# Kernel optimization log

Measured on AMD Instinct MI355X. Metric: run time of the kernel, lower is better.

The kernel has to match this reference:

```python
import jax, jax.numpy as jnp
import numpy as np

H = 256          # encoder hidden per direction
D = 2 * H        # decoder hidden / bidirectional feature dim
IN = 2
OUT = 2
B = 64
T = 256
STEPS = 24       # hard-coded decoder loop length in the source


def gru_cell(x, h, Wih, Whh, bih, bhh):
    # PyTorch GRU cell: gate order (r, z, n)
    gi = x @ Wih.T + bih
    gh = h @ Whh.T + bhh
    ir, iz, inn = jnp.split(gi, 3, axis=-1)
    hr, hz, hn = jnp.split(gh, 3, axis=-1)
    r = jax.nn.sigmoid(ir + hr)
    z = jax.nn.sigmoid(iz + hz)
    n = jnp.tanh(inn + r * hn)
    return (1.0 - z) * n + z * h


def run_dir(xs, Wih, Whh, bih, bhh, reverse):
    # xs: (T, B, F) time-major; returns outputs (T, B, H) and last hidden (B, H)
    h0 = jnp.zeros((xs.shape[1], Whh.shape[-1]), xs.dtype)
    def step(h, xt):
        h2 = gru_cell(xt, h, Wih, Whh, bih, bhh)
        return h2, h2
    h_last, ys = jax.lax.scan(step, h0, xs, reverse=reverse)
    return ys, h_last


def setup_inputs():
    keys = jax.random.split(jax.random.key(0), 24)
    k = iter(keys)
    def rn(shape, s):
        return jax.random.normal(next(k), shape, jnp.float32) * s
    se = 1.0 / np.sqrt(H)
    sd = 1.0 / np.sqrt(D)
    return {
        "x": rn((B, T, IN), 1.0),
        "enc_Wih0": rn((2, 3 * H, IN), se),
        "enc_Whh0": rn((2, 3 * H, H), se),
        "enc_bih0": rn((2, 3 * H), se),
        "enc_bhh0": rn((2, 3 * H), se),
        "enc_Wih": rn((2, 2, 3 * H, D), se),
        "enc_Whh": rn((2, 2, 3 * H, H), se),
        "enc_bih": rn((2, 2, 3 * H), se),
        "enc_bhh": rn((2, 2, 3 * H), se),
        "dec_Wih": rn((3, 3 * D, D), sd),
        "dec_Whh": rn((3, 3 * D, D), sd),
        "dec_bih": rn((3, 3 * D), sd),
        "dec_bhh": rn((3, 3 * D), sd),
        "fc_con_W": rn((D, 2 * D), sd),
        "fc_con_b": rn((D,), sd),
        "attn_W": rn((D, 2 * D), sd),
        "attn_b": rn((D,), sd),
        "v": jax.random.uniform(next(k), (D,), jnp.float32),  # torch.rand init
        "fc_W": rn((OUT, D), sd),
        "fc_b": rn((OUT,), sd),
    }


def reference(x, enc_Wih0, enc_Whh0, enc_bih0, enc_bhh0,
              enc_Wih, enc_Whh, enc_bih, enc_bhh,
              dec_Wih, dec_Whh, dec_bih, dec_bhh,
              fc_con_W, fc_con_b, attn_W, attn_b, v, fc_W, fc_b):
    # ---- bidirectional 3-layer GRU encoder ----
    seq = x.transpose(1, 0, 2)  # (T, B, IN) time-major
    hf_list, hb_list = [], []
    for l in range(3):
        if l == 0:
            Wf, Uf, bf, cf = enc_Wih0[0], enc_Whh0[0], enc_bih0[0], enc_bhh0[0]
            Wb, Ub, bb, cb = enc_Wih0[1], enc_Whh0[1], enc_bih0[1], enc_bhh0[1]
        else:
            Wf, Uf, bf, cf = enc_Wih[l-1, 0], enc_Whh[l-1, 0], enc_bih[l-1, 0], enc_bhh[l-1, 0]
            Wb, Ub, bb, cb = enc_Wih[l-1, 1], enc_Whh[l-1, 1], enc_bih[l-1, 1], enc_bhh[l-1, 1]
        yf, hf = run_dir(seq, Wf, Uf, bf, cf, False)
        yb, hb = run_dir(seq, Wb, Ub, bb, cb, True)
        seq = jnp.concatenate([yf, yb], axis=-1)
        hf_list.append(hf)
        hb_list.append(hb)
    enc_out = seq.transpose(1, 0, 2)  # (B, T, D)
    # hidden_decoder = cat(forward, backward) per layer -> (3, B, D)
    hidden = jnp.stack([jnp.concatenate([f, b], axis=-1)
                        for f, b in zip(hf_list, hb_list)])
    dec_in = enc_out[:, -1, :]  # (B, D)

    # additive attention: energy = tanh(W [h; enc_out] + b); precompute enc part
    attn_Wh = attn_W[:, :D]
    attn_We = attn_W[:, D:]
    enc_proj = jnp.einsum('bte,de->btd', enc_out, attn_We)  # (B, T, D)

    def dec_step(carry, _):
        d_in, hid = carry
        hq = hid[-1] @ attn_Wh.T                               # (B, D)
        energy = jnp.tanh(hq[:, None, :] + enc_proj + attn_b)  # (B, T, D)
        scores = jnp.einsum('btd,d->bt', energy, v)
        aw = jax.nn.softmax(scores, axis=1)                    # (B, T)
        ctx = jnp.einsum('bt,btd->bd', aw, enc_out)            # (B, D)
        inp = jnp.concatenate([d_in, ctx], axis=-1) @ fc_con_W.T + fc_con_b
        new_h = []
        for l in range(3):  # 3-layer unidirectional decoder GRU, single step
            hl = gru_cell(inp, hid[l], dec_Wih[l], dec_Whh[l], dec_bih[l], dec_bhh[l])
            new_h.append(hl)
            inp = hl
        out_step = inp @ fc_W.T + fc_b
        return (inp, jnp.stack(new_h)), out_step

    _, outs = jax.lax.scan(dec_step, (dec_in, hidden), None, length=STEPS)
    return outs.transpose(1, 0, 2)  # (B, 24, OUT)
```

## Files before the change

### kernel.cpp

```cpp
#include <hip/hip_runtime.h>

typedef unsigned short u16;
typedef unsigned int u32;
typedef _Float16 f16;
typedef f16   f16x2 __attribute__((ext_vector_type(2)));
typedef f16   f16x4 __attribute__((ext_vector_type(4)));
typedef f16   f16x8 __attribute__((ext_vector_type(8)));
typedef float f32x4 __attribute__((ext_vector_type(4)));

#define MFMA16(a,b,c) __builtin_amdgcn_mfma_f32_16x16x32_f16((a),(b),(c),0,0,0)

__device__ __forceinline__ float sigm_(float x){ return 1.f/(1.f + __expf(-x)); }
__device__ __forceinline__ float tanh_(float x){ return 1.f - 2.f/(1.f + __expf(2.f*x)); }
__device__ __forceinline__ float clampf(float x, float c){
  if (!(x > -c)) x = -c;
  if (x > c) x = c;
  return x;
}
__device__ __forceinline__ f16x8 cvt8f(const float* p){
  const float4 a = *(const float4*)p;
  const float4 b = *(const float4*)(p+4);
  f16x8 r;
  r[0]=(f16)a.x; r[1]=(f16)a.y; r[2]=(f16)a.z; r[3]=(f16)a.w;
  r[4]=(f16)b.x; r[5]=(f16)b.y; r[6]=(f16)b.z; r[7]=(f16)b.w;
  return r;
}

__device__ __forceinline__ void gbar8_(u32* c){
  __syncthreads();
  __threadfence();
  if (threadIdx.x == 0) {
    __hip_atomic_fetch_add(c, 1u, __ATOMIC_RELAXED, __HIP_MEMORY_SCOPE_AGENT);
    while (__hip_atomic_load(c, __ATOMIC_RELAXED, __HIP_MEMORY_SCOPE_AGENT) < 8u)
      __builtin_amdgcn_s_sleep(2);
  }
  __syncthreads();
  __threadfence();
}

__global__ void k_diag(float* out, int mib){
  const int i = blockIdx.x*256 + threadIdx.x;
  if (i < 3072) out[i] = 1000.f * (float)mib;
}

__global__ void k_prep_dec(const float* dWhh, const float* attnW, const float* fccon,
                           const float* dWih, f16* R3)
{
  long idx = (long)blockIdx.x*256 + threadIdx.x;
  const float* src; int rs, colOff = 0, NKS; long dst, loc;
  if (idx < 294912L) {
    loc = idx; const int m = (int)(loc / 98304); loc %= 98304;
    src = dWhh + (long)m*786432; rs = 512; NKS = 16; dst = (long)m*786432;
  } else if (idx < 327680L) {
    loc = idx - 294912L; src = attnW; colOff = 512; rs = 1024; NKS = 16; dst = 2359296L;
  } else if (idx < 393216L) {
    loc = idx - 327680L; src = fccon; rs = 1024; NKS = 32; dst = 2621440L;
  } else if (idx < 688128L) {
    loc = idx - 393216L; const int m = (int)(loc / 98304); loc %= 98304;
    src = dWih + (long)m*786432; rs = 512; NKS = 16; dst = 3440640L + (long)m*786432;
  } else if (idx < 720896L) {
    loc = idx - 688128L; src = attnW; colOff = 0; rs = 1024; NKS = 16; dst = 5799936L;
  } else return;
  const int lane = (int)(loc & 63);
  const long frag = loc >> 6;
  const int ks = (int)(frag % NKS);
  const long nt = frag / NKS;
  const int n  = (int)(nt*16 + (lane & 15));
  const int k0 = ks*32 + ((lane >> 4) << 3);
  const float* sp = src + (long)n*rs + colOff + k0;
  f16* dp = R3 + dst + loc*8;
  #pragma unroll
  for (int j = 0; j < 8; ++j) dp[j] = (f16)sp[j];
}

__global__ void k_gi0s(const float* __restrict__ x, const float* __restrict__ W,
                       const float* __restrict__ bi, f16* __restrict__ gi,
                       int seg, int BH, int lbh, int b0)
{
  const long idx = (long)blockIdx.x*256 + threadIdx.x;
  const int v = (int)(idx % 24);
  long rest = idx / 24;
  const int tid = (int)(rest & 511); rest >>= 9;
  const int bq = (int)(rest & ((1 << (lbh-4)) - 1)); rest >>= (lbh-4);
  const int s = (int)(rest & 63);
  const int d = (int)(rest >> 6);
  const int r = v / 6, rem = v % 6, i = rem / 3, g = rem % 3;
  const int w = tid >> 6, q = (tid >> 4) & 3, lo = tid & 15;
  const int n = g*256 + (2*w + i)*16 + lo;
  const int b = bq*16 + q*4 + r;
  const int t = d ? (255 - (seg*64 + s)) : (seg*64 + s);
  const float x0 = x[(((b0+b)<<8) + t)*2];
  const float x1 = x[(((b0+b)<<8) + t)*2 + 1];
  const long wi = ((long)d*768 + n)*2;
  gi[idx] = (f16)clampf(x0*W[wi] + x1*W[wi+1] + bi[d*768 + n], 32.f);
}

#define GIE(G, vv) ((float)((vv) < 8 ? (G)[0][(vv)&7] : ((vv) < 16 ? (G)[1][(vv)-8] : (G)[2][(vv)-16])))

__global__ __launch_bounds__(512, 1) void k_enc_seg(
    const f16* __restrict__ gi, const float* __restrict__ Wraw,
    const float* __restrict__ bhh, f16* __restrict__ seq, int ostr,
    f16* __restrict__ fin, float* __restrict__ hcar, int seg, int BH)
{
  const int tid = threadIdx.x;
  const int w = tid >> 6, lane = tid & 63;
  const int lo16 = lane & 15, quad = lane >> 4;
  const int nbq = BH >> 4;
  const int dir = blockIdx.x / nbq, bq = blockIdx.x % nbq;

  __shared__ f16 h16[4][16][264];

  const float* mat = Wraw + (long)dir*196608;
  f16x8 wr[6][8];
  #pragma unroll
  for (int p = 0; p < 3; ++p)
    #pragma unroll
    for (int i = 0; i < 2; ++i) {
      const int n = (p*16 + 2*w + i)*16 + lo16;
      #pragma unroll
      for (int ks = 0; ks < 8; ++ks)
        wr[p*2+i][ks] = cvt8f(mat + (long)n*256 + ks*32 + quad*8);
    }
  float bh_[3][2];
  #pragma unroll
  for (int p = 0; p < 3; ++p)
    #pragma unroll
    for (int i = 0; i < 2; ++i)
      bh_[p][i] = bhh[dir*768 + p*256 + (2*w+i)*16 + lo16];

  float hreg[2][4];
  if (seg == 0) {
    #pragma unroll
    for (int i = 0; i < 2; ++i)
      #pragma unroll
      for (int r = 0; r < 4; ++r) {
        hreg[i][r] = 0.f;
        h16[0][quad*4 + r][(2*w+i)*16 + lo16] = (f16)0.f;
      }
  } else {
    #pragma unroll
    for (int i = 0; i < 2; ++i) {
      const int c = (2*w+i)*16 + lo16;
      #pragma unroll
      for (int r = 0; r < 4; ++r) {
        const float v = hcar[((dir*BH) + bq*16 + quad*4 + r)*256 + c];
        hreg[i][r] = v;
        h16[0][quad*4 + r][c] = (f16)v;
      }
    }
  }

  const long gstep = (long)nbq*512*24;
  const f16* gbase = gi + (((long)dir*64*nbq + bq)*512 + tid)*24;
  f16x8 g0[3], g1[3];
  { const f16x8* gp = (const f16x8*)gbase; g0[0]=gp[0]; g0[1]=gp[1]; g0[2]=gp[2]; }

  const int frow = tid >> 5;
  const int fcol = (tid & 31) * 8;

  for (int s = 0; s < 64; ++s) {
    __syncthreads();
    if (s >= 2) {
      const int so = s - 2;
      const int t2 = dir ? (255 - (seg*64 + so)) : (seg*64 + so);
      const f16x8 hv = *(const f16x8*)&h16[(so+1)&3][frow][fcol];
      *(f16x8*)&seq[((long)t2*ostr + bq*16 + frow)*512 + dir*256 + fcol] = hv;
    }
    f32x4 acc[6];
    #pragma unroll
    for (int q = 0; q < 6; ++q) acc[q] = (f32x4){0.f,0.f,0.f,0.f};
    #pragma unroll
    for (int ks = 0; ks < 8; ++ks) {
      const f16x8 a = *(const f16x8*)&h16[s&3][lo16][ks*32 + quad*8];
      #pragma unroll
      for (int q = 0; q < 6; ++q)
        acc[q] = MFMA16(a, wr[q][ks], acc[q]);
    }
    if (s < 63) {
      const f16x8* gp = (const f16x8*)(gbase + (long)(s+1)*gstep);
      g1[0]=gp[0]; g1[1]=gp[1]; g1[2]=gp[2];
    }
    #pragma unroll
    for (int i = 0; i < 2; ++i) {
      const int c = (2*w+i)*16 + lo16;
      #pragma unroll
      for (int r = 0; r < 4; ++r) {
        const int row = quad*4 + r;
        const int v = r*6 + i*3;
        const float gir = GIE(g0, v);
        const float giz = GIE(g0, v+1);
        const float gin = GIE(g0, v+2);
        const float rv = sigm_(gir + acc[i][r]   + bh_[0][i]);
        const float zv = sigm_(giz + acc[2+i][r] + bh_[1][i]);
        const float nv = tanh_(gin + rv*(acc[4+i][r] + bh_[2][i]));
        float hn = (1.f - zv)*nv + zv*hreg[i][r];
        hn = clampf(hn, 2.f);
        hreg[i][r] = hn;
        h16[(s+1)&3][row][c] = (f16)hn;
        if (seg == 3 && s == 63) fin[(bq*16 + row)*512 + dir*256 + c] = (f16)hn;
      }
    }
    g0[0]=g1[0]; g0[1]=g1[1]; g0[2]=g1[2];
  }
  __syncthreads();
  #pragma unroll
  for (int so = 62; so < 64; ++so) {
    const int t2 = dir ? (255 - (seg*64 + so)) : (seg*64 + so);
    const f16x8 hv = *(const f16x8*)&h16[(so+1)&3][frow][fcol];
    *(f16x8*)&seq[((long)t2*ostr + bq*16 + frow)*512 + dir*256 + fcol] = hv;
  }
  #pragma unroll
  for (int i = 0; i < 2; ++i) {
    const int c = (2*w+i)*16 + lo16;
    #pragma unroll
    for (int r = 0; r < 4; ++r)
      hcar[((dir*BH) + bq*16 + quad*4 + r)*256 + c] = hreg[i][r];
  }
}

__global__ void k_gemm_gi(const f16* __restrict__ A,
                          const float* __restrict__ Braw, long bzs,
                          const float* __restrict__ bias,
                          f16* __restrict__ gi,
                          int tb0, int tb1, int tdirsgn, int abstr, float cv)
{
  const int tid = threadIdx.x, w = tid>>6, lane = tid&63;
  const int lo16 = lane&15, quad = lane>>4;
  const int s_ = blockIdx.x;
  const int y  = blockIdx.y;
  const int z  = blockIdx.z;
  const int tbase = z ? tb1 : tb0;
  const int tdir  = z ? -tdirsgn : tdirsgn;
  const int mrow = s_*64 + w*16 + lo16;
  const long arow = (long)(tbase + tdir*(mrow >> 6))*abstr + (mrow & 63);
  const f16* Ap = A + arow*512 + quad*8;
  const float* Bp = Braw + (long)z*bzs;
  f32x4 acc[12];
  #pragma unroll
  for (int i=0;i<12;++i) acc[i]=(f32x4){0.f,0.f,0.f,0.f};
  for (int ks = 0; ks < 16; ++ks) {
    const f16x8 a = *(const f16x8*)(Ap + ks*32);
    #pragma unroll
    for (int g = 0; g < 3; ++g)
      #pragma unroll
      for (int jj = 0; jj < 4; ++jj) {
        const int n = g*256 + y*64 + jj*16 + lo16;
        const f16x8 b = cvt8f(Bp + (long)n*512 + ks*32 + quad*8);
        acc[g*4+jj] = MFMA16(a, b, acc[g*4+jj]);
      }
  }
  f16* base = gi + (((long)z*64 + s_)*4 + w)*12288L;
  #pragma unroll
  for (int l = 0; l < 2; ++l) {
    f16x8 rec8[3];
    #pragma unroll
    for (int r = 0; r < 4; ++r)
      #pragma unroll
      for (int jl = 0; jl < 2; ++jl)
        #pragma unroll
        for (int g = 0; g < 3; ++g) {
          const int nt = g*4 + l*2 + jl;
          const int n = g*256 + y*64 + (l*2+jl)*16 + lo16;
          const int slot = r*6 + jl*3 + g;
          rec8[slot>>3][slot&7] = (f16)clampf(acc[nt][r] + bias[z*768 + n], cv);
        }
    f16* dp = base + ((long)(y*2 + l)*64 + quad*16 + lo16)*24L;
    *(f16x8*)(dp)      = rec8[0];
    *(f16x8*)(dp + 8)  = rec8[1];
    *(f16x8*)(dp + 16) = rec8[2];
  }
}

__global__ void k_gemm(const f16* __restrict__ A, int K,
                       const f16* __restrict__ Bsw, const float* __restrict__ Braw,
                       long bzs, int ldb, int koff,
                       const float* __restrict__ bias, int biaszs,
                       void* __restrict__ Cv, long czs, int ldc, int mode,
                       int tb0, int tb1, int tdirsgn, int lbh, int abstr, float cv)
{
  const int tid = threadIdx.x, w = tid>>6, lane = tid&63;
  const int lo16 = lane&15, quad = lane>>4;
  const int m0 = blockIdx.x*64 + w*16;
  const int n0 = blockIdx.y*128;
  const int z  = blockIdx.z;
  const int tbase = z ? tb1 : tb0;
  const int tdir  = z ? -tdirsgn : tdirsgn;
  const int NKS = K >> 5;
  const int mrow = m0 + lo16;
  const long arow = (long)(tbase + tdir*(mrow >> lbh))*abstr + (mrow & ((1<<lbh)-1));
  const f16* Ap = A + arow*K + quad*8;
  f32x4 acc[8];
  #pragma unroll
  for (int i=0;i<8;++i) acc[i]=(f32x4){0.f,0.f,0.f,0.f};
  if (Bsw) {
    const f16* Bp = Bsw + (long)z*bzs;
    for (int ks = 0; ks < NKS; ++ks) {
      const f16x8 a = *(const f16x8*)(Ap + ks*32);
      #pragma unroll
      for (int nt = 0; nt < 8; ++nt) {
        const f16x8 b = *(const f16x8*)(Bp + (((long)((n0>>4)+nt)*NKS + ks) << 9) + lane*8);
        acc[nt] = MFMA16(a, b, acc[nt]);
      }
    }
  } else {
    const float* Bp = Braw + (long)z*bzs;
    for (int ks = 0; ks < NKS; ++ks) {
      const f16x8 a = *(const f16x8*)(Ap + ks*32);
      #pragma unroll
      for (int nt = 0; nt < 8; ++nt) {
        const f16x8 b = cvt8f(Bp + (long)(n0 + nt*16 + lo16)*ldb + koff + ks*32 + quad*8);
        acc[nt] = MFMA16(a, b, acc[nt]);
      }
    }
  }
  #pragma unroll
  for (int nt = 0; nt < 8; ++nt) {
    const int n = n0 + nt*16 + lo16;
    const float bv = bias ? bias[z*biaszs + n] : 0.f;
    #pragma unroll
    for (int r = 0; r < 4; ++r) {
      const int m = m0 + quad*4 + r;
      const float val = clampf(acc[nt][r] + bv, cv);
      if (mode == 2) {
        const int s_ = m >> lbh, b_ = m & ((1<<lbh)-1);
        const int bq_ = b_ >> 4, q_ = (b_ >> 2) & 3, r_ = b_ & 3;
        const int g_ = n >> 8, j_ = (n >> 4) & 15, lo_ = n & 15;
        const long idx = ((((long)z*64 + s_)*(1<<(lbh-4)) + bq_)*512
                          + ((j_>>1)*64 + q_*16 + lo_))*24 + r_*6 + (j_&1)*3 + g_;
        ((f16*)Cv)[idx] = (f16)val;
      } else if (mode == 3)
        ((f16*)Cv)[(((long)(m & 63) << 8) + (m >> 6))*512 + n] = (f16)val;
      else if (mode == 1)
        ((f16*)Cv)[(long)z*czs + (long)m*ldc + n] = (f16)val;
      else
        ((float*)Cv)[(long)z*czs + (long)m*ldc + n] = val;
    }
  }
}

__global__ void k_score(const f16* __restrict__ seq, const f16* __restrict__ We,
                        const float* __restrict__ hq, const float* __restrict__ ab,
                        const float* __restrict__ vp, float* __restrict__ S)
{
  const int t = blockIdx.x, tid = threadIdx.x;
  const int w = tid>>6, lane = tid&63, lo16 = lane&15, quad = lane>>4;
  __shared__ float svab[1024];
  for (int i = tid; i < 512; i += 256) { svab[i] = vp[i]; svab[512+i] = ab[i]; }
  __syncthreads();
  f32x4 acc[32];
  #pragma unroll
  for (int i=0;i<32;++i) acc[i]=(f32x4){0.f,0.f,0.f,0.f};
  const f16* Ap = seq + ((long)t*64 + w*16 + lo16)*512 + quad*8;
  for (int ks = 0; ks < 16; ++ks) {
    const f16x8 a = *(const f16x8*)(Ap + ks*32);
    #pragma unroll
    for (int nt = 0; nt < 32; ++nt) {
      const f16x8 b = *(const f16x8*)(We + (((long)nt*16 + ks) << 9) + lane*8);
      acc[nt] = MFMA16(a, b, acc[nt]);
    }
  }
  #pragma unroll
  for (int r = 0; r < 4; ++r) {
    const int b = w*16 + quad*4 + r;
    float sc = 0.f;
    #pragma unroll
    for (int nt = 0; nt < 32; ++nt) {
      const int n = nt*16 + lo16;
      sc += svab[n] * tanh_(acc[nt][r] + hq[(b<<9) + n] + svab[512+n]);
    }
    sc += __shfl_xor(sc, 1, 64); sc += __shfl_xor(sc, 2, 64);
    sc += __shfl_xor(sc, 4, 64); sc += __shfl_xor(sc, 8, 64);
    if (lo16 == 0) S[(b<<8) + t] = clampf(sc, 256.f);
  }
}

__global__ void k_attnctx(const float* __restrict__ S, const f16* __restrict__ enc,
                          f16* __restrict__ cat)
{
  const int b = blockIdx.x, tid = threadIdx.x;
  __shared__ float ssc[256], srd[256];
  const float sc = clampf(S[(b<<8) + tid], 256.f);
  srd[tid] = sc; __syncthreads();
  for (int off = 128; off > 0; off >>= 1) { if (tid < off) srd[tid] = fmaxf(srd[tid], srd[tid+off]); __syncthreads(); }
  const float mx = srd[0]; __syncthreads();
  const float e = __expf(sc - mx);
  srd[tid] = e; __syncthreads();
  for (int off = 128; off > 0; off >>= 1) { if (tid < off) srd[tid] += srd[tid+off]; __syncthreads(); }
  const float inv = 1.f / srd[0]; __syncthreads();
  ssc[tid] = e * inv; __syncthreads();
  float c0 = 0.f, c1 = 0.f;
  for (int tt = 0; tt < 256; ++tt) {
    const float awt = ssc[tt];
    const f16* ep = enc + (((long)tt*64 + b) << 9);
    c0 += awt * (float)ep[tid];
    c1 += awt * (float)ep[256 + tid];
  }
  cat[(b<<10) + 512 + tid] = (f16)clampf(c0, 4.f);
  cat[(b<<10) + 768 + tid] = (f16)clampf(c1, 4.f);
}

__global__ void k_dec_init(const f16* __restrict__ fin, const f16* __restrict__ seq,
                           f16* __restrict__ hb16, float* __restrict__ hf32,
                           f16* __restrict__ cat, u32* __restrict__ cnt)
{
  const int idx = blockIdx.x*256 + threadIdx.x;
  if (idx < 3072) cnt[idx] = 0;
  const int d = idx & 511, b = (idx >> 9) & 63, l = idx >> 15;
  if (l < 3) {
    const float v = clampf((float)fin[((long)l<<15) + (b<<9) + d], 2.f);
    hb16[(long)l*65536 + (b<<9) + d] = (f16)v;
    hf32[(long)l*32768 + (b<<9) + d] = v;
  } else {
    cat[(b<<10) + d] = seq[((long)255*64 + b)*512 + d];
  }
}

__global__ __launch_bounds__(512, 1) void k_attn(
    const f16* __restrict__ seq, const f16* __restrict__ ep,
    const float* __restrict__ hf2, const f16* __restrict__ cat,
    const f16* __restrict__ whsw, const f16* __restrict__ fcsw,
    const float* __restrict__ fcconB, const float* __restrict__ vp,
    f16* __restrict__ inp, const float* __restrict__ fcW,
    const float* __restrict__ fcb, float* __restrict__ out, int step)
{
  const int b = blockIdx.x;
  const int tid = threadIdx.x, w = tid >> 6, lane = tid & 63;
  const int quad = lane >> 4;
  __shared__ float hsm[512];
  __shared__ float cats[1024];
  __shared__ float hqs[512];
  __shared__ float aw[256];
  __shared__ float red[8*512];
  hsm[tid]  = hf2[(b<<9) + tid];
  cats[tid] = (float)cat[(b<<10) + tid];
  __syncthreads();
  if (w < 2 && step > 0) {
    float p = 0.f;
    #pragma unroll
    for (int j = 0; j < 8; ++j) p += fcW[(w<<9) + lane*8 + j] * hsm[lane*8 + j];
    p += __shfl_xor(p,1,64); p += __shfl_xor(p,2,64); p += __shfl_xor(p,4,64);
    p += __shfl_xor(p,8,64); p += __shfl_xor(p,16,64); p += __shfl_xor(p,32,64);
    if (lane == 0) out[(b*24 + step-1)*2 + w] = clampf(p + fcb[w], 128.f);
  }
  #pragma unroll
  for (int i = 0; i < 4; ++i) {
    const int nt = w*4 + i;
    float p = 0.f;
    for (int ks = 0; ks < 16; ++ks) {
      const f16x8 wv = *(const f16x8*)(whsw + (((long)nt*16 + ks)<<9) + lane*8);
      const float4 ha = *(const float4*)&hsm[ks*32 + quad*8];
      const float4 hb = *(const float4*)&hsm[ks*32 + quad*8 + 4];
      p += (float)wv[0]*ha.x + (float)wv[1]*ha.y + (float)wv[2]*ha.z + (float)wv[3]*ha.w
         + (float)wv[4]*hb.x + (float)wv[5]*hb.y + (float)wv[6]*hb.z + (float)wv[7]*hb.w;
    }
    p += __shfl_xor(p,16,64); p += __shfl_xor(p,32,64);
    if (lane < 16) hqs[nt*16 + lane] = p;
  }
  __syncthreads();
  float hq8[8], v8[8];
  #pragma unroll
  for (int j = 0; j < 8; ++j) { hq8[j] = hqs[lane*8+j]; v8[j] = vp[lane*8+j]; }
  #pragma unroll 2
  for (int i = 0; i < 32; ++i) {
    const int t = w*32 + i;
    const f16x8 e = *(const f16x8*)(ep + (((long)(b<<8) + t)<<9) + lane*8);
    float s = 0.f;
    #pragma unroll
    for (int j = 0; j < 8; ++j) s += v8[j]*tanh_((float)e[j] + hq8[j]);
    s += __shfl_xor(s,1,64); s += __shfl_xor(s,2,64); s += __shfl_xor(s,4,64);
    s += __shfl_xor(s,8,64); s += __shfl_xor(s,16,64); s += __shfl_xor(s,32,64);
    if (lane == 0) aw[t] = clampf(s, 256.f);
  }
  __syncthreads();
  if (tid < 64) {
    float s0=aw[tid], s1=aw[tid+64], s2=aw[tid+128], s3=aw[tid+192];
    float mx = fmaxf(fmaxf(s0,s1), fmaxf(s2,s3));
    mx = fmaxf(mx, __shfl_xor(mx,1,64)); mx = fmaxf(mx, __shfl_xor(mx,2,64));
    mx = fmaxf(mx, __shfl_xor(mx,4,64)); mx = fmaxf(mx, __shfl_xor(mx,8,64));
    mx = fmaxf(mx, __shfl_xor(mx,16,64)); mx = fmaxf(mx, __shfl_xor(mx,32,64));
    const float e0=__expf(s0-mx), e1=__expf(s1-mx), e2=__expf(s2-mx), e3=__expf(s3-mx);
    float sm = e0+e1+e2+e3;
    sm += __shfl_xor(sm,1,64); sm += __shfl_xor(sm,2,64); sm += __shfl_xor(sm,4,64);
    sm += __shfl_xor(sm,8,64); sm += __shfl_xor(sm,16,64); sm += __shfl_xor(sm,32,64);
    const float inv = 1.f/sm;
    aw[tid]=e0*inv; aw[tid+64]=e1*inv; aw[tid+128]=e2*inv; aw[tid+192]=e3*inv;
  }
  __syncthreads();
  float c8[8];
  #pragma unroll
  for (int j = 0; j < 8; ++j) c8[j] = 0.f;
  #pragma unroll 2
  for (int i = 0; i < 32; ++i) {
    const int t = w*32 + i;
    const f16x8 e = *(const f16x8*)(seq + (((long)t*64 + b)<<9) + lane*8);
    const float awt = aw[t];
    #pragma unroll
    for (int j = 0; j < 8; ++j) c8[j] += awt*(float)e[j];
  }
  #pragma unroll
  for (int j = 0; j < 8; ++j) red[(w<<9) + lane*8 + j] = c8[j];
  __syncthreads();
  {
    float s = 0.f;
    #pragma unroll
    for (int ww = 0; ww < 8; ++ww) s += red[(ww<<9) + tid];
    cats[512 + tid] = clampf(s, 4.f);
  }
  __syncthreads();
  #pragma unroll
  for (int i = 0; i < 4; ++i) {
    const int nt = w*4 + i;
    float p = 0.f;
    for (int ks = 0; ks < 32; ++ks) {
      const f16x8 wv = *(const f16x8*)(fcsw + (((long)nt*32 + ks)<<9) + lane*8);
      const float4 ca = *(const float4*)&cats[ks*32 + quad*8];
      const float4 cb = *(const float4*)&cats[ks*32 + quad*8 + 4];
      p += (float)wv[0]*ca.x + (float)wv[1]*ca.y + (float)wv[2]*ca.z + (float)wv[3]*ca.w
         + (float)wv[4]*cb.x + (float)wv[5]*cb.y + (float)wv[6]*cb.z + (float)wv[7]*cb.w;
    }
    p += __shfl_xor(p,16,64); p += __shfl_xor(p,32,64);
    if (lane < 16) inp[(b<<9) + nt*16 + lane] = (f16)clampf(p + fcconB[nt*16+lane], 64.f);
  }
}

__global__ void k_cell3(const f16* __restrict__ inp0, const f16* __restrict__ WihSw,
                        const f16* __restrict__ WhhSw, const float* __restrict__ bihA,
                        const float* __restrict__ bhhA, float* __restrict__ hfA,
                        f16* __restrict__ hb, f16* __restrict__ cat, int p, u32* cnt)
{
  const int tid = threadIdx.x, w = tid>>6, lane = tid&63;
  const int lo16 = lane&15, quad = lane>>4;
  const int Wt = ((int)blockIdx.x & 7)*4 + w;
  const int mi = (int)blockIdx.x >> 3;
  for (int l = 0; l < 3; ++l) {
    const f16* inp = (l == 0) ? inp0 : (hb + (long)(2*(l-1) + (1-p))*32768);
    const f16* WihL = WihSw + (long)l*786432;
    const f16* WhhL = WhhSw + (long)l*786432;
    const float* bih = bihA + l*1536;
    const float* bhh = bhhA + l*1536;
    float* hf32 = hfA + (long)l*32768;
    const f16* hin = hb + (long)(2*l + p)*32768;
    f16* hout = hb + (long)(2*l + (1-p))*32768;
    f16* catp = (l == 2) ? cat : (f16*)nullptr;

    f32x4 arz[2], an_[2];
    #pragma unroll
    for (int i=0;i<2;++i){ arz[i]=(f32x4){0.f,0.f,0.f,0.f}; an_[i]=(f32x4){0.f,0.f,0.f,0.f}; }
    #pragma unroll 4
    for (int kk = 0; kk < 16; ++kk) {
      const f16x8 b0 = *(const f16x8*)(WihL + (((long)Wt*16 + kk)<<9)      + lane*8);
      const f16x8 b1 = *(const f16x8*)(WihL + (((long)(32+Wt)*16 + kk)<<9) + lane*8);
      const f16x8 b2 = *(const f16x8*)(WihL + (((long)(64+Wt)*16 + kk)<<9) + lane*8);
      const f16x8 a = *(const f16x8*)&inp[((mi*16 + lo16)<<9) + kk*32 + quad*8];
      arz[0] = MFMA16(a, b0, arz[0]);
      arz[1] = MFMA16(a, b1, arz[1]);
      an_[0] = MFMA16(a, b2, an_[0]);
    }
    #pragma unroll 4
    for (int kk = 0; kk < 16; ++kk) {
      const f16x8 b0 = *(const f16x8*)(WhhL + (((long)Wt*16 + kk)<<9)      + lane*8);
      const f16x8 b1 = *(const f16x8*)(WhhL + (((long)(32+Wt)*16 + kk)<<9) + lane*8);
      const f16x8 b2 = *(const f16x8*)(WhhL + (((long)(64+Wt)*16 + kk)<<9) + lane*8);
      const f16x8 a = *(const f16x8*)&hin[((mi*16 + lo16)<<9) + kk*32 + quad*8];
      arz[0] = MFMA16(a, b0, arz[0]);
      arz[1] = MFMA16(a, b1, arz[1]);
      an_[1] = MFMA16(a, b2, an_[1]);
    }
    const int c = Wt*16 + lo16;
    const float brz0 = bih[c]     + bhh[c];
    const float brz1 = bih[512+c] + bhh[512+c];
    const float bin_ = bih[1024+c];
    const float bhn_ = bhh[1024+c];
    #pragma unroll
    for (int r = 0; r < 4; ++r) {
      const int row = mi*16 + quad*4 + r;
      const float rv = sigm_(clampf(arz[0][r],64.f) + brz0);
      const float zv = sigm_(clampf(arz[1][r],64.f) + brz1);
      const float nv = tanh_(clampf(an_[0][r],64.f) + bin_ + rv*(clampf(an_[1][r],64.f) + bhn_));
      const float ho = hf32[(row<<9) + c];
      float hn2 = (1.f - zv)*nv + zv*ho;
      hn2 = clampf(hn2, 2.f);
      hf32[(row<<9) + c] = hn2;
      hout[(row<<9) + c] = (f16)hn2;
      if (catp) catp[(row<<10) + c] = (f16)hn2;
    }
    if (l < 2) gbar8_(cnt + (l*4 + mi)*16);
  }
}

__global__ void k_cell_raw(const f16* __restrict__ inp, const float* __restrict__ WihRaw,
                           const f16* __restrict__ WhhSw, const float* __restrict__ bih,
                           const float* __restrict__ bhh, float* __restrict__ hf32,
                           const f16* __restrict__ hin, f16* __restrict__ hout,
                           f16* __restrict__ cat)
{
  const int tid = threadIdx.x, w = tid>>6, lane = tid&63;
  const int lo16 = lane&15, quad = lane>>4;
  const int Wt = blockIdx.x*4 + w;
  f32x4 arz[8], an_[8];
  #pragma unroll
  for (int i=0;i<8;++i){ arz[i]=(f32x4){0.f,0.f,0.f,0.f}; an_[i]=(f32x4){0.f,0.f,0.f,0.f}; }
  const int nr = Wt*16 + lo16;
  const float* Rr = WihRaw + (long)nr*512        + quad*8;
  const float* Rz = WihRaw + (long)(512+nr)*512  + quad*8;
  const float* Rn = WihRaw + (long)(1024+nr)*512 + quad*8;
  #pragma unroll 2
  for (int kk = 0; kk < 16; ++kk) {
    const f16x8 b0 = cvt8f(Rr + kk*32);
    const f16x8 b1 = cvt8f(Rz + kk*32);
    const f16x8 b2 = cvt8f(Rn + kk*32);
    #pragma unroll
    for (int mi = 0; mi < 4; ++mi) {
      const f16x8 a = *(const f16x8*)&inp[((mi*16 + lo16)<<9) + kk*32 + quad*8];
      arz[mi]   = MFMA16(a, b0, arz[mi]);
      arz[4+mi] = MFMA16(a, b1, arz[4+mi]);
      an_[mi]   = MFMA16(a, b2, an_[mi]);
    }
  }
  #pragma unroll 2
  for (int kk = 0; kk < 16; ++kk) {
    const f16x8 b0 = *(const f16x8*)(WhhSw + (((long)Wt*16 + kk)<<9)      + lane*8);
    const f16x8 b1 = *(const f16x8*)(WhhSw + (((long)(32+Wt)*16 + kk)<<9) + lane*8);
    const f16x8 b2 = *(const f16x8*)(WhhSw + (((long)(64+Wt)*16 + kk)<<9) + lane*8);
    #pragma unroll
    for (int mi = 0; mi < 4; ++mi) {
      const f16x8 a = *(const f16x8*)&hin[((mi*16 + lo16)<<9) + kk*32 + quad*8];
      arz[mi]   = MFMA16(a, b0, arz[mi]);
      arz[4+mi] = MFMA16(a, b1, arz[4+mi]);
      an_[4+mi] = MFMA16(a, b2, an_[4+mi]);
    }
  }
  const int c = Wt*16 + lo16;
  const float brz0 = bih[c]     + bhh[c];
  const float brz1 = bih[512+c] + bhh[512+c];
  const float bin_ = bih[1024+c];
  const float bhn_ = bhh[1024+c];
  #pragma unroll
  for (int mi = 0; mi < 4; ++mi)
    #pragma unroll
    for (int r = 0; r < 4; ++r) {
      const int row = mi*16 + quad*4 + r;
      const float rv = sigm_(clampf(arz[mi][r],64.f)   + brz0);
      const float zv = sigm_(clampf(arz[4+mi][r],64.f) + brz1);
      const float nv = tanh_(clampf(an_[mi][r],64.f) + bin_ + rv*(clampf(an_[4+mi][r],64.f) + bhn_));
      const float ho = hf32[(row<<9) + c];
      float hn2 = (1.f - zv)*nv + zv*ho;
      hn2 = clampf(hn2, 2.f);
      hf32[(row<<9) + c] = hn2;
      hout[(row<<9) + c] = (f16)hn2;
      if (cat) cat[(row<<10) + c] = (f16)hn2;
    }
}

__global__ void k_out(const float* __restrict__ h2, const float* __restrict__ fcW,
                      const float* __restrict__ fcb, float* __restrict__ out, int step)
{
  const int b = blockIdx.x, t = threadIdx.x;
  __shared__ float r0[256], r1[256];
  const float ha = clampf(h2[(b<<9) + t], 2.f);
  const float hb = clampf(h2[(b<<9) + 256 + t], 2.f);
  r0[t] = ha*fcW[t]     + hb*fcW[256+t];
  r1[t] = ha*fcW[512+t] + hb*fcW[768+t];
  __syncthreads();
  for (int off = 128; off > 0; off >>= 1) {
    if (t < off) { r0[t] += r0[t+off]; r1[t] += r1[t+off]; }
    __syncthreads();
  }
  if (t == 0) {
    out[(b*24 + step)*2]     = clampf(r0[0] + fcb[0], 128.f);
    out[(b*24 + step)*2 + 1] = clampf(r1[0] + fcb[1], 128.f);
  }
}

extern "C" void kernel_launch(void* const* d_in, const int* in_sizes, int n_in,
                              void* d_out, int out_size, void* d_ws, size_t ws_size,
                              hipStream_t stream) {
  const float* X      = (const float*)d_in[0];
  const float* eWih0  = (const float*)d_in[1];
  const float* eWhh0  = (const float*)d_in[2];
  const float* ebih0  = (const float*)d_in[3];
  const float* ebhh0  = (const float*)d_in[4];
  const float* eWih   = (const float*)d_in[5];
  const float* eWhh   = (const float*)d_in[6];
  const float* ebih   = (const float*)d_in[7];
  const float* ebhh   = (const float*)d_in[8];
  const float* dWih   = (const float*)d_in[9];
  const float* dWhh   = (const float*)d_in[10];
  const float* dbih   = (const float*)d_in[11];
  const float* dbhh   = (const float*)d_in[12];
  const float* fcconW = (const float*)d_in[13];
  const float* fcconB = (const float*)d_in[14];
  const float* attnW  = (const float*)d_in[15];
  const float* attnB  = (const float*)d_in[16];
  const float* vW     = (const float*)d_in[17];
  const float* fcW    = (const float*)d_in[18];
  const float* fcB    = (const float*)d_in[19];
  float* OUT = (float*)d_out;

  const long need_big  = 47054848L;
  const long need_half = 32964608L;
  f16* H = (f16*)d_ws;
  f16 *SEQ = H, *L1OUT, *GIB, *R3, *FIN, *HB, *CAT, *INP;
  float *HC;
  int BH, lbh, nh, l1ostr, l1abstr; long gdir;

  if ((long)ws_size >= need_big) {
    BH = 64; lbh = 6; nh = 1; l1ostr = 64; l1abstr = 64;
    L1OUT = H + 8388608L;
    GIB   = H + 16777216L;
    HC    = (float*)(H + 23068672L);
    FIN   = H + 23134208L;
    HB    = H + 23232512L;
    CAT   = H + 23429120L;
    INP   = H + 23494656L;
    gdir  = 3145728L;
  } else if ((long)ws_size >= need_half) {
    BH = 32; lbh = 5; nh = 2; l1ostr = 32; l1abstr = 32;
    L1OUT = H + 8388608L;
    GIB   = H + 12582912L;
    HC    = (float*)(H + 16023552L);
    FIN   = H + 16089088L;
    HB    = H + 16187392L;
    CAT   = H + 16384000L;
    INP   = H + 16449536L;
    gdir  = 1572864L;
  } else {
    k_diag<<<12, 256, 0, stream>>>(OUT, (int)(ws_size >> 20));
    return;
  }
  R3 = GIB;
  float* ST = (float*)(GIB + 3145728L);
  float* HQ = ST;
  float* HF = ST + 32768;
  float* S  = ST + 131072;
  u32* CNT = (u32*)ST;
  const int nblk = 2*(BH>>4);
  const int gi0grid = (2*64*BH*768)/256;

  for (int h = 0; h < nh; ++h) {
    const int b0 = h*BH;
    for (int seg = 0; seg < 4; ++seg) {
      k_gi0s<<<gi0grid, 256, 0, stream>>>(X, eWih0, ebih0, GIB, seg, BH, lbh, b0);
      k_enc_seg<<<nblk, 512, 0, stream>>>(GIB, eWhh0, ebhh0, SEQ + (long)b0*512, 64,
                                          FIN + (long)b0*512, HC, seg, BH);
    }
    for (int seg = 0; seg < 4; ++seg) {
      if (BH == 64)
        k_gemm_gi<<<dim3(64, 4, 2), 256, 0, stream>>>(SEQ, eWih, 393216L, ebih,
            GIB, seg*64, 255 - seg*64, 1, 64, 32.f);
      else
        k_gemm<<<dim3(BH, 6, 2), 256, 0, stream>>>(SEQ + (long)b0*512, 512,
            (const f16*)nullptr, eWih, 393216L, 512, 0, ebih, 768,
            GIB, gdir, 768, 2, seg*64, 255 - seg*64, 1, lbh, 64, 32.f);
      k_enc_seg<<<nblk, 512, 0, stream>>>(GIB, eWhh, ebhh, L1OUT, l1ostr,
                                          FIN + 32768 + (long)b0*512, HC, seg, BH);
    }
    for (int seg = 0; seg < 4; ++seg) {
      if (BH == 64)
        k_gemm_gi<<<dim3(64, 4, 2), 256, 0, stream>>>(L1OUT, eWih + 2L*393216,
            393216L, ebih + 1536, GIB, seg*64, 255 - seg*64, 1, 64, 32.f);
      else
        k_gemm<<<dim3(BH, 6, 2), 256, 0, stream>>>(L1OUT, 512,
            (const f16*)nullptr, eWih + 2L*393216, 393216L, 512, 0, ebih + 1536, 768,
            GIB, gdir, 768, 2, seg*64, 255 - seg*64, 1, lbh, l1abstr, 32.f);
      k_enc_seg<<<nblk, 512, 0, stream>>>(GIB, eWhh + 2L*196608, ebhh + 1536,
                                          SEQ + (long)b0*512, 64,
                                          FIN + 65536 + (long)b0*512, HC, seg, BH);
    }
  }

  if (BH == 64) {
    f16* EP    = L1OUT;
    f16* WIHSW = GIB + 3440640L;
    f16* WHSW  = GIB + 5799936L;

    k_prep_dec<<<2816, 256, 0, stream>>>(dWhh, attnW, fcconW, dWih, R3);
    k_gemm<<<dim3(256, 4, 1), 256, 0, stream>>>(SEQ, 512,
        R3 + 2359296L, (const float*)nullptr, 0L, 0, 0, attnB, 0,
        EP, 0L, 512, 3, 0, 0, 1, 6, 64, 32.f);
    k_dec_init<<<512, 256, 0, stream>>>(FIN, SEQ, HB, HF, CAT, CNT);

    for (int s = 0; s < 24; ++s) {
      const int p = s & 1;
      k_attn<<<64, 512, 0, stream>>>(SEQ, EP, HF + 2*32768, CAT, WHSW, R3 + 2621440L,
          fcconB, vW, INP, fcW, fcB, OUT, s);
      k_cell3<<<32, 256, 0, stream>>>(INP, WIHSW, R3, dbih, dbhh, HF, HB, CAT,
          p, CNT + s*128);
    }
    k_out<<<64, 256, 0, stream>>>(HF + 2*32768, fcW, fcB, OUT, 23);
  } else {
    k_prep_dec<<<1536, 256, 0, stream>>>(dWhh, attnW, fcconW, dWih, R3);
    k_dec_init<<<512, 256, 0, stream>>>(FIN, SEQ, HB, HF, CAT, (u32*)(S + 16000));

    for (int s = 0; s < 24; ++s) {
      const int p = s & 1;
      const f16* h2in = HB + (4 + p)*32768L;
      k_gemm<<<dim3(1,4,1), 256, 0, stream>>>(h2in, 512,
          (const f16*)nullptr, attnW, 0L, 1024, 0, (const float*)nullptr, 0,
          HQ, 0L, 512, 0, 0, 0, 0, 6, 64, 64.f);
      k_score<<<256, 256, 0, stream>>>(SEQ, R3 + 2359296L, HQ, attnB, vW, S);
      k_attnctx<<<64, 256, 0, stream>>>(S, SEQ, CAT);
      k_gemm<<<dim3(1,4,1), 256, 0, stream>>>(CAT, 1024,
          R3 + 2621440L, (const float*)nullptr, 0L, 0, 0, fcconB, 0,
          INP, 0L, 512, 1, 0, 0, 0, 6, 64, 64.f);
      for (int l = 0; l < 3; ++l) {
        const f16* inp = (l == 0) ? INP : (HB + (2*(l-1) + (1-p))*32768L);
        k_cell_raw<<<8, 256, 0, stream>>>(inp,
                  dWih + (long)l*786432, R3 + (long)l*786432,
                  dbih + l*1536, dbhh + l*1536, HF + (long)l*32768,
                  HB + (2*l + p)*32768L, HB + (2*l + (1-p))*32768L,
                  (l == 2) ? CAT : (f16*)nullptr);
      }
      k_out<<<64, 256, 0, stream>>>(HF + 2*32768, fcW, fcB, OUT, s);
    }
  }
}
```

Baseline: 6.061 ms.

## Fuse encoder recurrence with next-chunk input projection in one launch

```diff
diff --git a/kernel.cpp b/kernel.cpp
--- a/kernel.cpp
+++ b/kernel.cpp
@@ -218,56 +218,217 @@
   }
 }
 
-__global__ void k_gemm_gi(const f16* __restrict__ A,
-                          const float* __restrict__ Braw, long bzs,
-                          const float* __restrict__ bias,
-                          f16* __restrict__ gi,
-                          int tb0, int tb1, int tdirsgn, int abstr, float cv)
-{
-  const int tid = threadIdx.x, w = tid>>6, lane = tid&63;
-  const int lo16 = lane&15, quad = lane>>4;
-  const int s_ = blockIdx.x;
-  const int y  = blockIdx.y;
-  const int z  = blockIdx.z;
-  const int tbase = z ? tb1 : tb0;
-  const int tdir  = z ? -tdirsgn : tdirsgn;
-  const int mrow = s_*64 + w*16 + lo16;
-  const long arow = (long)(tbase + tdir*(mrow >> 6))*abstr + (mrow & 63);
-  const f16* Ap = A + arow*512 + quad*8;
-  const float* Bp = Braw + (long)z*bzs;
-  f32x4 acc[12];
-  #pragma unroll
-  for (int i=0;i<12;++i) acc[i]=(f32x4){0.f,0.f,0.f,0.f};
-  for (int ks = 0; ks < 16; ++ks) {
-    const f16x8 a = *(const f16x8*)(Ap + ks*32);
-    #pragma unroll
-    for (int g = 0; g < 3; ++g)
-      #pragma unroll
-      for (int jj = 0; jj < 4; ++jj) {
-        const int n = g*256 + y*64 + jj*16 + lo16;
-        const f16x8 b = cvt8f(Bp + (long)n*512 + ks*32 + quad*8);
-        acc[g*4+jj] = MFMA16(a, b, acc[g*4+jj]);
-      }
-  }
-  f16* base = gi + (((long)z*64 + s_)*4 + w)*12288L;
-  #pragma unroll
-  for (int l = 0; l < 2; ++l) {
-    f16x8 rec8[3];
-    #pragma unroll
-    for (int r = 0; r < 4; ++r)
-      #pragma unroll
-      for (int jl = 0; jl < 2; ++jl)
+__global__ __launch_bounds__(512, 1) void k_enc_f(
+    const f16* __restrict__ giC, f16* __restrict__ giP,
+    const float* __restrict__ Wraw, const float* __restrict__ bhh,
+    f16* __restrict__ seq, f16* __restrict__ fin, float* __restrict__ hcar,
+    int hs, int encOn, int prodMode, int ht,
+    const float* __restrict__ xin, const float* __restrict__ Wih0,
+    const float* __restrict__ bih0,
+    const f16* __restrict__ Asrc, const float* __restrict__ Braw,
+    const float* __restrict__ bias)
+{
+  __shared__ f16 h16[4][16][264];
+  const int tid = threadIdx.x;
+  const int bid = blockIdx.x;
+
+  if (encOn && bid < 8) {
+    const int w = tid >> 6, lane = tid & 63;
+    const int lo16 = lane & 15, quad = lane >> 4;
+    const int dir = bid >> 2, bq = bid & 3;
+
+    const float* mat = Wraw + (long)dir*196608;
+    f16x8 wr[6][8];
+    #pragma unroll
+    for (int p = 0; p < 3; ++p)
+      #pragma unroll
+      for (int i = 0; i < 2; ++i) {
+        const int n = (p*16 + 2*w + i)*16 + lo16;
+        #pragma unroll
+        for (int ks = 0; ks < 8; ++ks)
+          wr[p*2+i][ks] = cvt8f(mat + (long)n*256 + ks*32 + quad*8);
+      }
+    float bh_[3][2];
+    #pragma unroll
+    for (int p = 0; p < 3; ++p)
+      #pragma unroll
+      for (int i = 0; i < 2; ++i)
+        bh_[p][i] = bhh[dir*768 + p*256 + (2*w+i)*16 + lo16];
+
+    float hreg[2][4];
+    if (hs == 0) {
+      #pragma unroll
+      for (int i = 0; i < 2; ++i)
+        #pragma unroll
+        for (int r = 0; r < 4; ++r) {
+          hreg[i][r] = 0.f;
+          h16[0][quad*4 + r][(2*w+i)*16 + lo16] = (f16)0.f;
+        }
+    } else {
+      #pragma unroll
+      for (int i = 0; i < 2; ++i) {
+        const int c = (2*w+i)*16 + lo16;
+        #pragma unroll
+        for (int r = 0; r < 4; ++r) {
+          const float v = hcar[((dir*64) + bq*16 + quad*4 + r)*256 + c];
+          hreg[i][r] = v;
+          h16[0][quad*4 + r][c] = (f16)v;
+        }
+      }
+    }
+
+    const long gstep = 4L*512*24;
+    const f16* gbase = giC + (((long)dir*32*4 + bq)*512 + tid)*24;
+    f16x8 g0[3], g1[3];
+    { const f16x8* gp = (const f16x8*)gbase; g0[0]=gp[0]; g0[1]=gp[1]; g0[2]=gp[2]; }
+
+    const int frow = tid >> 5;
+    const int fcol = (tid & 31) * 8;
+
+    for (int s = 0; s < 32; ++s) {
+      __syncthreads();
+      if (s >= 2) {
+        const int so = s - 2;
+        const int t2 = dir ? (255 - (hs*32 + so)) : (hs*32 + so);
+        const f16x8 hv = *(const f16x8*)&h16[(so+1)&3][frow][fcol];
+        *(f16x8*)&seq[((long)t2*64 + bq*16 + frow)*512 + dir*256 + fcol] = hv;
+      }
+      f32x4 acc[6];
+      #pragma unroll
+      for (int q = 0; q < 6; ++q) acc[q] = (f32x4){0.f,0.f,0.f,0.f};
+      #pragma unroll
+      for (int ks = 0; ks < 8; ++ks) {
+        const f16x8 a = *(const f16x8*)&h16[s&3][lo16][ks*32 + quad*8];
+        #pragma unroll
+        for (int q = 0; q < 6; ++q)
+          acc[q] = MFMA16(a, wr[q][ks], acc[q]);
+      }
+      if (s < 31) {
+        const f16x8* gp = (const f16x8*)(gbase + (long)(s+1)*gstep);
+        g1[0]=gp[0]; g1[1]=gp[1]; g1[2]=gp[2];
+      }
+      #pragma unroll
+      for (int i = 0; i < 2; ++i) {
+        const int c = (2*w+i)*16 + lo16;
+        #pragma unroll
+        for (int r = 0; r < 4; ++r) {
+          const int row = quad*4 + r;
+          const int v = r*6 + i*3;
+          const float gir = GIE(g0, v);
+          const float giz = GIE(g0, v+1);
+          const float gin = GIE(g0, v+2);
+          const float rv = sigm_(gir + acc[i][r]   + bh_[0][i]);
+          const float zv = sigm_(giz + acc[2+i][r] + bh_[1][i]);
+          const float nv = tanh_(gin + rv*(acc[4+i][r] + bh_[2][i]));
+          float hn = (1.f - zv)*nv + zv*hreg[i][r];
+          hn = clampf(hn, 2.f);
+          hreg[i][r] = hn;
+          h16[(s+1)&3][row][c] = (f16)hn;
+          if (hs == 7 && s == 31) fin[(bq*16 + row)*512 + dir*256 + c] = (f16)hn;
+        }
+      }
+      g0[0]=g1[0]; g0[1]=g1[1]; g0[2]=g1[2];
+    }
+    __syncthreads();
+    #pragma unroll
+    for (int so = 30; so < 32; ++so) {
+      const int t2 = dir ? (255 - (hs*32 + so)) : (hs*32 + so);
+      const f16x8 hv = *(const f16x8*)&h16[(so+1)&3][frow][fcol];
+      *(f16x8*)&seq[((long)t2*64 + bq*16 + frow)*512 + dir*256 + fcol] = hv;
+    }
+    #pragma unroll
+    for (int i = 0; i < 2; ++i) {
+      const int c = (2*w+i)*16 + lo16;
+      #pragma unroll
+      for (int r = 0; r < 4; ++r)
+        hcar[((dir*64) + bq*16 + quad*4 + r)*256 + c] = hreg[i][r];
+    }
+    return;
+  }
+
+  const int pb = bid - (encOn ? 8 : 0);
+  if (prodMode == 1) {
+    const int u = pb*512 + tid;
+    const int tid9 = u & 511;
+    const int bq = (u >> 9) & 3;
+    const int s  = (u >> 11) & 31;
+    const int d  = u >> 16;
+    const int w = tid9 >> 6, q = (tid9 >> 4) & 3, lo = tid9 & 15;
+    float wv0[2][3], wv1[2][3], bv[2][3];
+    #pragma unroll
+    for (int i = 0; i < 2; ++i)
+      #pragma unroll
+      for (int g = 0; g < 3; ++g) {
+        const int n = g*256 + (2*w + i)*16 + lo;
+        const long wi = ((long)d*768 + n)*2;
+        wv0[i][g] = Wih0[wi];
+        wv1[i][g] = Wih0[wi + 1];
+        bv[i][g]  = bih0[d*768 + n];
+      }
+    f16x8 rec[3];
+    #pragma unroll
+    for (int r = 0; r < 4; ++r) {
+      const int b = bq*16 + q*4 + r;
+      const int t = d ? (255 - (ht*32 + s)) : (ht*32 + s);
+      const float x0 = xin[((b<<8) + t)*2];
+      const float x1 = xin[((b<<8) + t)*2 + 1];
+      #pragma unroll
+      for (int i = 0; i < 2; ++i)
         #pragma unroll
         for (int g = 0; g < 3; ++g) {
-          const int nt = g*4 + l*2 + jl;
-          const int n = g*256 + y*64 + (l*2+jl)*16 + lo16;
-          const int slot = r*6 + jl*3 + g;
-          rec8[slot>>3][slot&7] = (f16)clampf(acc[nt][r] + bias[z*768 + n], cv);
+          const int slot = r*6 + i*3 + g;
+          rec[slot>>3][slot&7] = (f16)clampf(x0*wv0[i][g] + x1*wv1[i][g] + bv[i][g], 32.f);
         }
-    f16* dp = base + ((long)(y*2 + l)*64 + quad*16 + lo16)*24L;
-    *(f16x8*)(dp)      = rec8[0];
-    *(f16x8*)(dp + 8)  = rec8[1];
-    *(f16x8*)(dp + 16) = rec8[2];
+    }
+    f16* dp = giP + ((((long)d*32 + s)*4 + bq)*512 + tid9)*24;
+    *(f16x8*)(dp)      = rec[0];
+    *(f16x8*)(dp + 8)  = rec[1];
+    *(f16x8*)(dp + 16) = rec[2];
+  } else if (prodMode == 2) {
+    const int s2 = pb & 15, y = (pb >> 4) & 3, z = pb >> 6;
+    const int sub = tid >> 8, stid = tid & 255;
+    const int s_ = s2*2 + sub;
+    const int w4 = stid >> 6, lane = stid & 63;
+    const int lo16 = lane & 15, quad = lane >> 4;
+    const int tb = z ? (255 - ht*32) : (ht*32);
+    const int td = z ? -1 : 1;
+    const long arow = (long)(tb + td*s_)*64 + (w4*16 + lo16);
+    const f16* Ap = Asrc + arow*512 + quad*8;
+    const float* Bp = Braw + (long)z*393216;
+    f32x4 acc[12];
+    #pragma unroll
+    for (int i=0;i<12;++i) acc[i]=(f32x4){0.f,0.f,0.f,0.f};
+    for (int ks = 0; ks < 16; ++ks) {
+      const f16x8 a = *(const f16x8*)(Ap + ks*32);
+      #pragma unroll
+      for (int g = 0; g < 3; ++g)
+        #pragma unroll
+        for (int jj = 0; jj < 4; ++jj) {
+          const int n = g*256 + y*64 + jj*16 + lo16;
+          const f16x8 b = cvt8f(Bp + (long)n*512 + ks*32 + quad*8);
+          acc[g*4+jj] = MFMA16(a, b, acc[g*4+jj]);
+        }
+    }
+    f16* base = giP + (((long)z*32 + s_)*4 + w4)*12288L;
+    #pragma unroll
+    for (int l = 0; l < 2; ++l) {
+      f16x8 rec8[3];
+      #pragma unroll
+      for (int r = 0; r < 4; ++r)
+        #pragma unroll
+        for (int jl = 0; jl < 2; ++jl)
+          #pragma unroll
+          for (int g = 0; g < 3; ++g) {
+            const int nt = g*4 + l*2 + jl;
+            const int n = g*256 + y*64 + (l*2+jl)*16 + lo16;
+            const int slot = r*6 + jl*3 + g;
+            rec8[slot>>3][slot&7] = (f16)clampf(acc[nt][r] + bias[z*768 + n], 32.f);
+          }
+      f16* dp = base + ((long)(y*2 + l)*64 + quad*16 + lo16)*24L;
+      *(f16x8*)(dp)      = rec8[0];
+      *(f16x8*)(dp + 8)  = rec8[1];
+      *(f16x8*)(dp + 16) = rec8[2];
+    }
   }
 }
 
@@ -735,41 +896,40 @@
   float* S  = ST + 131072;
   u32* CNT = (u32*)ST;
   const int nblk = 2*(BH>>4);
-  const int gi0grid = (2*64*BH*768)/256;
-
-  for (int h = 0; h < nh; ++h) {
-    const int b0 = h*BH;
-    for (int seg = 0; seg < 4; ++seg) {
-      k_gi0s<<<gi0grid, 256, 0, stream>>>(X, eWih0, ebih0, GIB, seg, BH, lbh, b0);
-      k_enc_seg<<<nblk, 512, 0, stream>>>(GIB, eWhh0, ebhh0, SEQ + (long)b0*512, 64,
-                                          FIN + (long)b0*512, HC, seg, BH);
-    }
-    for (int seg = 0; seg < 4; ++seg) {
-      if (BH == 64)
-        k_gemm_gi<<<dim3(64, 4, 2), 256, 0, stream>>>(SEQ, eWih, 393216L, ebih,
-            GIB, seg*64, 255 - seg*64, 1, 64, 32.f);
-      else
-        k_gemm<<<dim3(BH, 6, 2), 256, 0, stream>>>(SEQ + (long)b0*512, 512,
-            (const f16*)nullptr, eWih, 393216L, 512, 0, ebih, 768,
-            GIB, gdir, 768, 2, seg*64, 255 - seg*64, 1, lbh, 64, 32.f);
-      k_enc_seg<<<nblk, 512, 0, stream>>>(GIB, eWhh, ebhh, L1OUT, l1ostr,
-                                          FIN + 32768 + (long)b0*512, HC, seg, BH);
-    }
-    for (int seg = 0; seg < 4; ++seg) {
-      if (BH == 64)
-        k_gemm_gi<<<dim3(64, 4, 2), 256, 0, stream>>>(L1OUT, eWih + 2L*393216,
-            393216L, ebih + 1536, GIB, seg*64, 255 - seg*64, 1, 64, 32.f);
-      else
-        k_gemm<<<dim3(BH, 6, 2), 256, 0, stream>>>(L1OUT, 512,
-            (const f16*)nullptr, eWih + 2L*393216, 393216L, 512, 0, ebih + 1536, 768,
-            GIB, gdir, 768, 2, seg*64, 255 - seg*64, 1, lbh, l1abstr, 32.f);
-      k_enc_seg<<<nblk, 512, 0, stream>>>(GIB, eWhh + 2L*196608, ebhh + 1536,
-                                          SEQ + (long)b0*512, 64,
-                                          FIN + 65536 + (long)b0*512, HC, seg, BH);
-    }
-  }
 
   if (BH == 64) {
+    f16* GI[2] = { GIB, GIB + 3145728L };
+    k_enc_f<<<256, 512, 0, stream>>>(GI[0], GI[0], eWhh0, ebhh0, SEQ, FIN, HC,
+        0, 0, 1, 0, X, eWih0, ebih0, (const f16*)nullptr, (const float*)nullptr,
+        (const float*)nullptr);
+    for (int h = 0; h < 8; ++h) {
+      const int prod = (h < 7) ? 1 : 0;
+      k_enc_f<<<8 + (prod ? 256 : 0), 512, 0, stream>>>(GI[h&1], GI[(h+1)&1],
+          eWhh0, ebhh0, SEQ, FIN, HC, h, 1, prod, h+1, X, eWih0, ebih0,
+          (const f16*)nullptr, (const float*)nullptr, (const float*)nullptr);
+    }
+    k_enc_f<<<128, 512, 0, stream>>>(GI[0], GI[0], eWhh, ebhh, L1OUT, FIN + 32768, HC,
+        0, 0, 2, 0, (const float*)nullptr, (const float*)nullptr, (const float*)nullptr,
+        SEQ, eWih, ebih);
+    for (int h = 0; h < 8; ++h) {
+      const int prod = (h < 7) ? 2 : 0;
+      k_enc_f<<<8 + (prod ? 128 : 0), 512, 0, stream>>>(GI[h&1], GI[(h+1)&1],
+          eWhh, ebhh, L1OUT, FIN + 32768, HC, h, 1, prod, h+1,
+          (const float*)nullptr, (const float*)nullptr, (const float*)nullptr,
+          SEQ, eWih, ebih);
+    }
+    k_enc_f<<<128, 512, 0, stream>>>(GI[0], GI[0], eWhh + 2L*196608, ebhh + 1536,
+        SEQ, FIN + 65536, HC, 0, 0, 2, 0,
+        (const float*)nullptr, (const float*)nullptr, (const float*)nullptr,
+        L1OUT, eWih + 2L*393216, ebih + 1536);
+    for (int h = 0; h < 8; ++h) {
+      const int prod = (h < 7) ? 2 : 0;
+      k_enc_f<<<8 + (prod ? 128 : 0), 512, 0, stream>>>(GI[h&1], GI[(h+1)&1],
+          eWhh + 2L*196608, ebhh + 1536, SEQ, FIN + 65536, HC, h, 1, prod, h+1,
+          (const float*)nullptr, (const float*)nullptr, (const float*)nullptr,
+          L1OUT, eWih + 2L*393216, ebih + 1536);
+    }
+
     f16* EP    = L1OUT;
     f16* WIHSW = GIB + 3440640L;
     f16* WHSW  = GIB + 5799936L;
@@ -789,6 +949,31 @@
     }
     k_out<<<64, 256, 0, stream>>>(HF + 2*32768, fcW, fcB, OUT, 23);
   } else {
+    const int gi0grid = (2*64*BH*768)/256;
+    for (int h = 0; h < nh; ++h) {
+      const int b0 = h*BH;
+      for (int seg = 0; seg < 4; ++seg) {
+        k_gi0s<<<gi0grid, 256, 0, stream>>>(X, eWih0, ebih0, GIB, seg, BH, lbh, b0);
+        k_enc_seg<<<nblk, 512, 0, stream>>>(GIB, eWhh0, ebhh0, SEQ + (long)b0*512, 64,
+                                            FIN + (long)b0*512, HC, seg, BH);
+      }
+      for (int seg = 0; seg < 4; ++seg) {
+        k_gemm<<<dim3(BH, 6, 2), 256, 0, stream>>>(SEQ + (long)b0*512, 512,
+            (const f16*)nullptr, eWih, 393216L, 512, 0, ebih, 768,
+            GIB, gdir, 768, 2, seg*64, 255 - seg*64, 1, lbh, 64, 32.f);
+        k_enc_seg<<<nblk, 512, 0, stream>>>(GIB, eWhh, ebhh, L1OUT, l1ostr,
+                                            FIN + 32768 + (long)b0*512, HC, seg, BH);
+      }
+      for (int seg = 0; seg < 4; ++seg) {
+        k_gemm<<<dim3(BH, 6, 2), 256, 0, stream>>>(L1OUT, 512,
+            (const f16*)nullptr, eWih + 2L*393216, 393216L, 512, 0, ebih + 1536, 768,
+            GIB, gdir, 768, 2, seg*64, 255 - seg*64, 1, lbh, l1abstr, 32.f);
+        k_enc_seg<<<nblk, 512, 0, stream>>>(GIB, eWhh + 2L*196608, ebhh + 1536,
+                                            SEQ + (long)b0*512, 64,
+                                            FIN + 65536 + (long)b0*512, HC, seg, BH);
+      }
+    }
+
     k_prep_dec<<<1536, 256, 0, stream>>>(dWhh, attnW, fcconW, dWih, R3);
     k_dec_init<<<512, 256, 0, stream>>>(FIN, SEQ, HB, HF, CAT, (u32*)(S + 16000));
 
```

New measurement: 5.843 ms. 1.04x faster.
